# Kernel tuning notes

Hardware: AMD Instinct MI355X
Metric: run time of the kernel (lower is better)

Reference implementation:

```python
import jax, jax.numpy as jnp
import numpy as np

OUT_FEATURES = 4096
IN_FEATURES = 4096
GROUP_SIZE = 128
NUM_GROUPS = OUT_FEATURES // GROUP_SIZE  # groups along output-channel axis (axis=0)


def _unpack_int8_to_int4(packed, num_elements):
    # Each int8 byte holds two signed int4 values: low nibble first, then high nibble.
    p = packed.astype(jnp.int8)
    low = jnp.right_shift(jnp.left_shift(p, 4), 4)   # sign-extended low nibble, in [-8, 7]
    high = jnp.right_shift(p, 4)                      # arithmetic shift -> sign-extended high nibble
    vals = jnp.stack([low, high], axis=-1).reshape(-1)
    return vals[:num_elements]


def _dequantize_weight(packed_weight, scales, zero_points):
    int4 = _unpack_int8_to_int4(packed_weight, OUT_FEATURES * IN_FEATURES)
    w = int4.astype(jnp.float32).reshape(NUM_GROUPS, GROUP_SIZE, IN_FEATURES)
    # per-group (over output channels): (q - zp) * scale
    w = (w - zero_points[:, None, None]) * scales[:, None, None]
    return w.reshape(OUT_FEATURES, IN_FEATURES)


def setup_inputs() -> dict:
    key = jax.random.key(0)
    k_x, k_w, k_s, k_zp, k_b = jax.random.split(key, 5)
    x = jax.random.normal(k_x, (8192, IN_FEATURES), dtype=jnp.float32)
    # packed int4 weights stored as signed bytes
    packed_weight = jax.random.randint(k_w, (OUT_FEATURES * IN_FEATURES // 2,), 0, 256, dtype=jnp.int32) - 128
    scales = jax.random.uniform(k_s, (NUM_GROUPS,), dtype=jnp.float32) * 0.02 + 0.001
    zero_points = jax.random.normal(k_zp, (NUM_GROUPS,), dtype=jnp.float32) * 0.5
    bias = jax.random.normal(k_b, (OUT_FEATURES,), dtype=jnp.float32)
    return {"x": x, "packed_weight": packed_weight, "scales": scales,
            "zero_points": zero_points, "bias": bias}


def reference(x, packed_weight, scales, zero_points, bias):
    weight = _dequantize_weight(packed_weight, scales, zero_points)  # [out, in]
    return jnp.einsum('bi,oi->bo', x, weight) + bias
```

## Files before the change

### kernel.cpp

```cpp
#include <hip/hip_runtime.h>
#include <cstdint>
#include <cstddef>

#define M_DIM 8192
#define N_DIM 4096
#define K_DIM 4096
#define CHUNK_M 4096

typedef __attribute__((ext_vector_type(8))) short bf16x8;
typedef __attribute__((ext_vector_type(4))) float floatx4;

__device__ __forceinline__ ushort f2bf_rne(float f) {
    union { float f; uint32_t u; } a;
    a.f = f;
    uint32_t u = a.u;
    uint32_t r = (u + 0x7fffu + ((u >> 16) & 1u)) >> 16;
    return (ushort)r;
}

__device__ __forceinline__ uint32_t pk_bf_trunc(float f0, float f1) {
    return __builtin_amdgcn_perm(__float_as_uint(f1), __float_as_uint(f0),
                                 0x07060302u);
}

__global__ void dequant_w_kernel(const int4* __restrict__ pw,
                                 const float* __restrict__ scales,
                                 const float* __restrict__ zps,
                                 uint4* __restrict__ wb, int np4) {
    int p4 = blockIdx.x * blockDim.x + threadIdx.x;
    if (p4 >= np4) return;
    int p = p4 * 4;
    int g = p >> 18;
    float s = scales[g];
    float b = -zps[g] * s;
    int4 v = pw[p4];
    int vv[4] = { v.x, v.y, v.z, v.w };
    ushort o[8];
#pragma unroll
    for (int j = 0; j < 4; ++j) {
        int lo = ((int)((uint32_t)vv[j] << 28)) >> 28;
        int hi = ((int)((uint32_t)vv[j] << 24)) >> 28;
        o[2 * j]     = f2bf_rne(fmaf((float)lo, s, b));
        o[2 * j + 1] = f2bf_rne(fmaf((float)hi, s, b));
    }
    uint4 st;
    st.x = (uint32_t)o[0] | ((uint32_t)o[1] << 16);
    st.y = (uint32_t)o[2] | ((uint32_t)o[3] << 16);
    st.z = (uint32_t)o[4] | ((uint32_t)o[5] << 16);
    st.w = (uint32_t)o[6] | ((uint32_t)o[7] << 16);
    wb[p4] = st;
}

__global__ void convert_x_kernel(const float4* __restrict__ x4,
                                 ushort4* __restrict__ out4, int n4) {
    int i = blockIdx.x * blockDim.x + threadIdx.x;
    if (i >= n4) return;
    float4 v = x4[i];
    ushort4 o;
    o.x = f2bf_rne(v.x);
    o.y = f2bf_rne(v.y);
    o.z = f2bf_rne(v.z);
    o.w = f2bf_rne(v.w);
    out4[i] = o;
}

#define TBM 256
#define TBN 256
#define TBK 32
#define NT  (K_DIM / TBK)
#define A_E 8192
#define SLOT_E 16384

__global__ __launch_bounds__(512, 2)
void gemm_bf16_256(const ushort* __restrict__ A,
                   const ushort* __restrict__ B,
                   const float* __restrict__ bias,
                   float* __restrict__ C) {
    __shared__ ushort lds[4 * SLOT_E];

    const int tid  = threadIdx.x;
    const int lane = tid & 63;
    const int wave = tid >> 6;
    const int wm   = wave >> 2;
    const int wn   = wave & 3;

    const int nwg = gridDim.x;
    const int cpx = nwg >> 3;
    const int bid = blockIdx.x;
    const int swz = (bid & 7) * cpx + (bid >> 3);
    const int bn  = swz & (N_DIM / TBN - 1);
    const int bm  = swz / (N_DIM / TBN);

    const ushort* Ab = A + (size_t)(bm * TBM) * K_DIM;
    const ushort* Bb = B + (size_t)(bn * TBN) * K_DIM;

    const int srow = tid >> 2;
    const int scol = (((tid & 3) ^ ((tid >> 3) & 3)) * 8);
    const ushort* gA0 = Ab + (size_t)srow * K_DIM + scol;
    const ushort* gA1 = gA0 + (size_t)128 * K_DIM;
    const ushort* gB0 = Bb + (size_t)srow * K_DIM + scol;
    const ushort* gB1 = gB0 + (size_t)128 * K_DIM;
    const int wdst = wave * 512;

    const int frow = lane & 15;
    const int fcol = (((lane >> 4) ^ ((frow >> 1) & 3)) * 8);
    const int aoff = (wm * 128 + frow) * TBK + fcol;
    const int boff = A_E + (wn * 64 + frow) * TBK + fcol;

    floatx4 acc[8][4] = {};

#define STAGE_A(tt)                                                           \
    {                                                                          \
        const int k0s = ((tt) & (NT - 1)) * TBK;                               \
        ushort* d = lds + ((tt) & 3) * SLOT_E + wdst;                          \
        __builtin_amdgcn_global_load_lds(                                      \
            (const __attribute__((address_space(1))) void*)(gA0 + k0s),        \
            (__attribute__((address_space(3))) void*)d, 16, 0, 0);             \
        __builtin_amdgcn_global_load_lds(                                      \
            (const __attribute__((address_space(1))) void*)(gA1 + k0s),        \
            (__attribute__((address_space(3))) void*)(d + 4096), 16, 0, 0);    \
    }
#define STAGE_B(tt)                                                           \
    {                                                                          \
        const int k0s = ((tt) & (NT - 1)) * TBK;                               \
        ushort* d = lds + ((tt) & 3) * SLOT_E + A_E + wdst;                    \
        __builtin_amdgcn_global_load_lds(                                      \
            (const __attribute__((address_space(1))) void*)(gB0 + k0s),        \
            (__attribute__((address_space(3))) void*)d, 16, 0, 0);             \
        __builtin_amdgcn_global_load_lds(                                      \
            (const __attribute__((address_space(1))) void*)(gB1 + k0s),        \
            (__attribute__((address_space(3))) void*)(d + 4096), 16, 0, 0);    \
    }

    STAGE_A(0) STAGE_B(0)
    STAGE_A(1) STAGE_B(1)
    STAGE_A(2) STAGE_B(2)
    asm volatile("s_waitcnt vmcnt(8)" ::: "memory");
    __builtin_amdgcn_s_barrier();
    __builtin_amdgcn_sched_barrier(0);

    for (int t = 0; t < NT; ++t) {
        const ushort* base = lds + (t & 3) * SLOT_E;

        bf16x8 bf[4], af[4];
#pragma unroll
        for (int j = 0; j < 4; ++j)
            bf[j] = *(const bf16x8*)(base + boff + j * 512);
#pragma unroll
        for (int i = 0; i < 4; ++i)
            af[i] = *(const bf16x8*)(base + aoff + i * 512);
        STAGE_A(t + 3)
        __builtin_amdgcn_s_barrier();
        asm volatile("s_waitcnt lgkmcnt(0)" ::: "memory");
        __builtin_amdgcn_sched_barrier(0);
        __builtin_amdgcn_s_setprio(1);
#pragma unroll
        for (int i = 0; i < 4; ++i)
#pragma unroll
            for (int j = 0; j < 4; ++j)
                acc[i][j] = __builtin_amdgcn_mfma_f32_16x16x32_bf16(
                    af[i], bf[j], acc[i][j], 0, 0, 0);
        __builtin_amdgcn_s_setprio(0);
        __builtin_amdgcn_s_barrier();
        __builtin_amdgcn_sched_barrier(0);

#pragma unroll
        for (int i = 0; i < 4; ++i)
            af[i] = *(const bf16x8*)(base + aoff + (4 + i) * 512);
        STAGE_B(t + 3)
        __builtin_amdgcn_s_barrier();
        asm volatile("s_waitcnt lgkmcnt(0)" ::: "memory");
        __builtin_amdgcn_sched_barrier(0);
        __builtin_amdgcn_s_setprio(1);
#pragma unroll
        for (int i = 0; i < 4; ++i)
#pragma unroll
            for (int j = 0; j < 4; ++j)
                acc[4 + i][j] = __builtin_amdgcn_mfma_f32_16x16x32_bf16(
                    af[i], bf[j], acc[4 + i][j], 0, 0, 0);
        __builtin_amdgcn_s_setprio(0);
        asm volatile("s_waitcnt vmcnt(8)" ::: "memory");
        __builtin_amdgcn_s_barrier();
        __builtin_amdgcn_sched_barrier(0);
    }
#undef STAGE_A
#undef STAGE_B

    const int crow0 = bm * TBM + wm * 128;
    const int ccol0 = bn * TBN + wn * 64;
    const int rl = lane >> 4;
    const int cl = lane & 15;
#pragma unroll
    for (int j = 0; j < 4; ++j) {
        const int col = ccol0 + j * 16 + cl;
        const float bv = bias[col];
#pragma unroll
        for (int i = 0; i < 8; ++i) {
            const int row = crow0 + i * 16 + rl * 4;
            float* cp = C + (size_t)row * N_DIM + col;
#pragma unroll
            for (int r = 0; r < 4; ++r)
                cp[(size_t)r * N_DIM] = acc[i][j][r] + bv;
        }
    }
}

#define BM 128
#define BN 128
#define BK 32

__global__ void gemm_fused_kernel(const float* __restrict__ X,
                                  const ushort* __restrict__ B,
                                  const float* __restrict__ bias,
                                  float* __restrict__ C) {
    __shared__ ushort As[BM * BK];
    __shared__ ushort Bs[BN * BK];

    const int tid  = threadIdx.x;
    const int lane = tid & 63;
    const int wave = tid >> 6;
    const int wm   = wave >> 1;
    const int wn   = wave & 1;
    const int bm   = blockIdx.y;
    const int bn   = blockIdx.x;

    const int ar = tid >> 2;
    const int ac = (tid & 3) * 8;
    const float* xp0 = X + (size_t)(bm * BM + ar) * K_DIM + ac;
    const float* xp1 = xp0 + (size_t)64 * K_DIM;
    ushort* as0 = As + ar * BK + ac;
    ushort* as1 = as0 + 64 * BK;

    const int scol = (lane & 3) * 8;
    const ushort* Bb = B + (size_t)(bn * BN) * K_DIM;

    floatx4 acc[4][4] = {};

    for (int k0 = 0; k0 < K_DIM; k0 += BK) {
        float4 a0 = *(const float4*)(xp0 + k0);
        float4 a1 = *(const float4*)(xp0 + k0 + 4);
        float4 b0 = *(const float4*)(xp1 + k0);
        float4 b1 = *(const float4*)(xp1 + k0 + 4);
#pragma unroll
        for (int q = 0; q < 2; ++q) {
            const int chunk = wave * 2 + q;
            const int r = chunk * 16 + (lane >> 2);
            const ushort* gb = Bb + (size_t)r * K_DIM + k0 + scol;
            __builtin_amdgcn_global_load_lds(
                (const __attribute__((address_space(1))) void*)gb,
                (__attribute__((address_space(3))) void*)(Bs + chunk * 512),
                16, 0, 0);
        }
        uint4 w0, w1;
        w0.x = pk_bf_trunc(a0.x, a0.y);
        w0.y = pk_bf_trunc(a0.z, a0.w);
        w0.z = pk_bf_trunc(a1.x, a1.y);
        w0.w = pk_bf_trunc(a1.z, a1.w);
        w1.x = pk_bf_trunc(b0.x, b0.y);
        w1.y = pk_bf_trunc(b0.z, b0.w);
        w1.z = pk_bf_trunc(b1.x, b1.y);
        w1.w = pk_bf_trunc(b1.z, b1.w);
        *(uint4*)as0 = w0;
        *(uint4*)as1 = w1;

        __syncthreads();

        bf16x8 af[4], bfr[4];
        const int frow = lane & 15;
        const int fcol = (lane >> 4) * 8;
#pragma unroll
        for (int i = 0; i < 4; ++i) {
            af[i]  = *(const bf16x8*)(As + (wm * 64 + i * 16 + frow) * BK + fcol);
            bfr[i] = *(const bf16x8*)(Bs + (wn * 64 + i * 16 + frow) * BK + fcol);
        }
#pragma unroll
        for (int i = 0; i < 4; ++i)
#pragma unroll
            for (int j = 0; j < 4; ++j)
                acc[i][j] = __builtin_amdgcn_mfma_f32_16x16x32_bf16(
                    af[i], bfr[j], acc[i][j], 0, 0, 0);
        __syncthreads();
    }

    const int crow0 = bm * BM + wm * 64;
    const int ccol0 = bn * BN + wn * 64;
    const int rl = lane >> 4;
    const int cl = lane & 15;
#pragma unroll
    for (int j = 0; j < 4; ++j) {
        const int col = ccol0 + j * 16 + cl;
        const float bv = bias[col];
#pragma unroll
        for (int i = 0; i < 4; ++i) {
            const int row = crow0 + i * 16 + rl * 4;
            float* cp = C + (size_t)row * N_DIM + col;
#pragma unroll
            for (int r = 0; r < 4; ++r)
                cp[(size_t)r * N_DIM] = acc[i][j][r] + bv;
        }
    }
}

extern "C" void kernel_launch(void* const* d_in, const int* in_sizes, int n_in,
                              void* d_out, int out_size, void* d_ws, size_t ws_size,
                              hipStream_t stream) {
    const float* x      = (const float*)d_in[0];
    const int*   pw     = (const int*)d_in[1];
    const float* scales = (const float*)d_in[2];
    const float* zps    = (const float*)d_in[3];
    const float* bias   = (const float*)d_in[4];
    float* out = (float*)d_out;

    ushort* wb = (ushort*)d_ws;

    {
        int np4 = (N_DIM * K_DIM / 2) / 4;
        dequant_w_kernel<<<np4 / 256, 256, 0, stream>>>(
            (const int4*)pw, scales, zps, (uint4*)wb, np4);
    }

    const size_t need = ((size_t)N_DIM * K_DIM + (size_t)CHUNK_M * K_DIM) * 2;
    if (ws_size >= need) {
        ushort* xb = wb + (size_t)N_DIM * K_DIM;
        for (int c = 0; c < M_DIM / CHUNK_M; ++c) {
            const float* xc = x + (size_t)c * CHUNK_M * K_DIM;
            float* oc = out + (size_t)c * CHUNK_M * N_DIM;
            int n4 = (CHUNK_M * K_DIM) / 4;
            convert_x_kernel<<<n4 / 256, 256, 0, stream>>>(
                (const float4*)xc, (ushort4*)xb, n4);
            int nblk = (CHUNK_M / TBM) * (N_DIM / TBN);
            gemm_bf16_256<<<nblk, 512, 0, stream>>>(xb, wb, bias, oc);
        }
    } else {
        dim3 grid(N_DIM / BN, M_DIM / BM);
        gemm_fused_kernel<<<grid, 256, 0, stream>>>(x, wb, bias, out);
    }
}
```

Baseline: 483.8 us.

## Software-pipeline LDS fragment loads and launch single full-M GEMM

Restructures the GEMM main loop into a two-way unrolled ping-pong that prefetches the next tile's A/B fragments from LDS while MFMAs on the current tile run. Both global-to-LDS stages are issued at the start of each iteration, and the per-iteration barrier count drops from four to one. The vmcnt wait changes to match the new issue order. It also adds a path that converts all of x at once and launches one GEMM over the full M when the workspace is large enough, removing the chunk loop's extra launches and tail effects. This raises register pressure and workspace use, and the reduced synchronization around LDS slot reuse needs care.

New measurement: 472.5 us. 1.02x faster.

```diff
diff --git a/kernel.cpp b/kernel.cpp
--- a/kernel.cpp
+++ b/kernel.cpp
@@ -132,57 +132,62 @@
             (__attribute__((address_space(3))) void*)(d + 4096), 16, 0, 0);    \
     }
 
+#define BODY(T, afc, bfc, afn, bfn)                                           \
+    {                                                                          \
+        STAGE_A((T) + 3) STAGE_B((T) + 3)                                      \
+        const ushort* bcur = lds + ((T) & 3) * SLOT_E;                         \
+        const ushort* bnxt = lds + (((T) + 1) & 3) * SLOT_E;                   \
+        bf16x8 afb[4];                                                         \
+        _Pragma("unroll")                                                      \
+        for (int i = 0; i < 4; ++i)                                            \
+            afb[i] = *(const bf16x8*)(bcur + aoff + (4 + i) * 512);            \
+        __builtin_amdgcn_s_setprio(1);                                         \
+        _Pragma("unroll")                                                      \
+        for (int i = 0; i < 4; ++i)                                            \
+            _Pragma("unroll")                                                  \
+            for (int j = 0; j < 4; ++j)                                        \
+                acc[i][j] = __builtin_amdgcn_mfma_f32_16x16x32_bf16(           \
+                    afc[i], bfc[j], acc[i][j], 0, 0, 0);                       \
+        __builtin_amdgcn_s_setprio(0);                                         \
+        _Pragma("unroll")                                                      \
+        for (int j = 0; j < 4; ++j)                                            \
+            bfn[j] = *(const bf16x8*)(bnxt + boff + j * 512);                  \
+        _Pragma("unroll")                                                      \
+        for (int i = 0; i < 4; ++i)                                            \
+            afn[i] = *(const bf16x8*)(bnxt + aoff + i * 512);                  \
+        __builtin_amdgcn_s_setprio(1);                                         \
+        _Pragma("unroll")                                                      \
+        for (int i = 0; i < 4; ++i)                                            \
+            _Pragma("unroll")                                                  \
+            for (int j = 0; j < 4; ++j)                                        \
+                acc[4 + i][j] = __builtin_amdgcn_mfma_f32_16x16x32_bf16(       \
+                    afb[i], bfc[j], acc[4 + i][j], 0, 0, 0);                   \
+        __builtin_amdgcn_s_setprio(0);                                         \
+        asm volatile("s_waitcnt vmcnt(4)" ::: "memory");                       \
+        __builtin_amdgcn_s_barrier();                                          \
+        __builtin_amdgcn_sched_barrier(0);                                     \
+    }
+
     STAGE_A(0) STAGE_B(0)
     STAGE_A(1) STAGE_B(1)
     STAGE_A(2) STAGE_B(2)
-    asm volatile("s_waitcnt vmcnt(8)" ::: "memory");
+    asm volatile("s_waitcnt vmcnt(4)" ::: "memory");
     __builtin_amdgcn_s_barrier();
     __builtin_amdgcn_sched_barrier(0);
 
-    for (int t = 0; t < NT; ++t) {
-        const ushort* base = lds + (t & 3) * SLOT_E;
-
-        bf16x8 bf[4], af[4];
-#pragma unroll
-        for (int j = 0; j < 4; ++j)
-            bf[j] = *(const bf16x8*)(base + boff + j * 512);
-#pragma unroll
-        for (int i = 0; i < 4; ++i)
-            af[i] = *(const bf16x8*)(base + aoff + i * 512);
-        STAGE_A(t + 3)
-        __builtin_amdgcn_s_barrier();
-        asm volatile("s_waitcnt lgkmcnt(0)" ::: "memory");
-        __builtin_amdgcn_sched_barrier(0);
-        __builtin_amdgcn_s_setprio(1);
-#pragma unroll
-        for (int i = 0; i < 4; ++i)
-#pragma unroll
-            for (int j = 0; j < 4; ++j)
-                acc[i][j] = __builtin_amdgcn_mfma_f32_16x16x32_bf16(
-                    af[i], bf[j], acc[i][j], 0, 0, 0);
-        __builtin_amdgcn_s_setprio(0);
-        __builtin_amdgcn_s_barrier();
-        __builtin_amdgcn_sched_barrier(0);
-
-#pragma unroll
-        for (int i = 0; i < 4; ++i)
-            af[i] = *(const bf16x8*)(base + aoff + (4 + i) * 512);
-        STAGE_B(t + 3)
-        __builtin_amdgcn_s_barrier();
-        asm volatile("s_waitcnt lgkmcnt(0)" ::: "memory");
-        __builtin_amdgcn_sched_barrier(0);
-        __builtin_amdgcn_s_setprio(1);
-#pragma unroll
-        for (int i = 0; i < 4; ++i)
-#pragma unroll
-            for (int j = 0; j < 4; ++j)
-                acc[4 + i][j] = __builtin_amdgcn_mfma_f32_16x16x32_bf16(
-                    af[i], bf[j], acc[4 + i][j], 0, 0, 0);
-        __builtin_amdgcn_s_setprio(0);
-        asm volatile("s_waitcnt vmcnt(8)" ::: "memory");
-        __builtin_amdgcn_s_barrier();
-        __builtin_amdgcn_sched_barrier(0);
-    }
+    bf16x8 af0[4], bf0[4], af1[4], bf1[4];
+#pragma unroll
+    for (int j = 0; j < 4; ++j)
+        bf0[j] = *(const bf16x8*)(lds + boff + j * 512);
+#pragma unroll
+    for (int i = 0; i < 4; ++i)
+        af0[i] = *(const bf16x8*)(lds + aoff + i * 512);
+
+    for (int t = 0; t < NT; t += 2) {
+        BODY(t,     af0, bf0, af1, bf1)
+        BODY(t + 1, af1, bf1, af0, bf0)
+    }
+#undef BODY
 #undef STAGE_A
 #undef STAGE_B
 
@@ -319,8 +324,17 @@
             (const int4*)pw, scales, zps, (uint4*)wb, np4);
     }
 
-    const size_t need = ((size_t)N_DIM * K_DIM + (size_t)CHUNK_M * K_DIM) * 2;
-    if (ws_size >= need) {
+    const size_t need_full  = ((size_t)N_DIM * K_DIM + (size_t)M_DIM * K_DIM) * 2;
+    const size_t need_chunk = ((size_t)N_DIM * K_DIM + (size_t)CHUNK_M * K_DIM) * 2;
+
+    if (ws_size >= need_full) {
+        ushort* xb = wb + (size_t)N_DIM * K_DIM;
+        int n4 = (M_DIM * K_DIM) / 4;
+        convert_x_kernel<<<n4 / 256, 256, 0, stream>>>(
+            (const float4*)x, (ushort4*)xb, n4);
+        int nblk = (M_DIM / TBM) * (N_DIM / TBN);
+        gemm_bf16_256<<<nblk, 512, 0, stream>>>(xb, wb, bias, out);
+    } else if (ws_size >= need_chunk) {
         ushort* xb = wb + (size_t)N_DIM * K_DIM;
         for (int c = 0; c < M_DIM / CHUNK_M; ++c) {
             const float* xc = x + (size_t)c * CHUNK_M * K_DIM;
```
